# Optimization experiments

Measured on AMD Instinct MI355X. Metric: run time of the kernel, lower is better.

## Reference

```python
import jax, jax.numpy as jnp
import numpy as np

B = 4096
D = 256
N = 9000000
ALPHA = 0.5      # alpha_weight
GAMMA_S = 0.8
GAMMA_U = 0.9
RHO = 6.0
EPS = 1e-14
ETA = 0.01
TAU_MIN = 0.001
TAU_MAX = 1.0
GRAD_CLIP = 5.0
TAU_INIT = 0.07


def setup_inputs() -> dict:
    key = jax.random.key(0)
    k1, k2 = jax.random.split(key)
    return {
        "zis": jax.random.normal(k1, (B, D), dtype=jnp.float32),
        "zjs": jax.random.normal(k2, (B, D), dtype=jnp.float32),
        "ids": jnp.arange(B, dtype=jnp.int32),
        "s_I": jnp.zeros(N, jnp.float32),
        "s_T": jnp.zeros(N, jnp.float32),
        "b_I": jnp.zeros(N, jnp.float32),
        "b_T": jnp.zeros(N, jnp.float32),
        "u_I": jnp.zeros(N, jnp.float32),
        "u_T": jnp.zeros(N, jnp.float32),
        "tau_I": jnp.full(N, TAU_INIT, jnp.float32),
        "tau_T": jnp.full(N, TAU_INIT, jnp.float32),
    }


def reference(zis, zjs, ids, s_I, s_T, b_I, b_T, u_I, u_T, tau_I, tau_T):
    sg = jax.lax.stop_gradient
    Bc = zis.shape[0]
    # normalize
    zis = zis / jnp.linalg.norm(zis, axis=1, keepdims=True)
    zjs = zjs / jnp.linalg.norm(zjs, axis=1, keepdims=True)
    sim = jnp.einsum('id,jd->ij', zis, zjs)                 # [B,B]
    diag = jnp.diagonal(sim)
    image_diffs = sim - diag[:, None]
    text_diffs = sim - diag[None, :]
    tau_i = tau_I[ids]
    tau_t = tau_T[ids]
    # detached temperature-scaled diffs (torch .detach())
    idt = sg(image_diffs) / tau_i[:, None]
    tdt = sg(text_diffs) / tau_t[None, :]
    # running max update (online log-sum-exp shift)
    old_b_i = b_I[ids]
    old_b_t = b_T[ids]
    new_b_i = jnp.maximum(old_b_i, idt.max(axis=1))
    new_b_t = jnp.maximum(old_b_t, tdt.max(axis=0))
    mask = 1.0 - jnp.eye(Bc, dtype=zis.dtype)
    exp_i = jnp.exp(idt - new_b_i[:, None]) * mask
    exp_t = jnp.exp(tdt - new_b_t[None, :]) * mask
    g_i = exp_i.sum(axis=1)                                  # [B]
    g_t = exp_t.sum(axis=0)                                  # [B]
    # EMA of normalizers, rescaled by max shift
    s_i = (1.0 - GAMMA_S) * s_I[ids] * jnp.exp(old_b_i - new_b_i) + GAMMA_S * g_i
    s_t = (1.0 - GAMMA_S) * s_T[ids] * jnp.exp(old_b_t - new_b_t) + GAMMA_S * g_t
    s_i_c = jnp.clip(s_i, EPS, None)[:, None]                # [B,1]
    s_t_c = jnp.clip(s_t, EPS, None)[None, :]                # [1,B]
    w_i = exp_i / s_i_c
    w_t = exp_t / s_t_c
    image_loss = (sg(w_i) * image_diffs).sum(axis=1)         # [B]
    text_loss = (sg(w_t) * text_diffs).sum(axis=0)           # [B]
    total_loss = ALPHA * image_loss.mean() + (1.0 - ALPHA) * text_loss.mean()
    grad_tau_image = jnp.log(s_i_c) + new_b_i[:, None] + RHO - (w_i * idt).sum(axis=1, keepdims=True) / (Bc - 1)
    grad_tau_text = jnp.log(s_t_c) + new_b_t[None, :] + RHO - (w_t * tdt).sum(axis=0, keepdims=True) / (Bc - 1)
    # EMA of tau gradients with clipping, then temperature update
    u_i = (1.0 - GAMMA_U) * u_I[ids] + GAMMA_U * jnp.clip(grad_tau_image[:, 0], -GRAD_CLIP, GRAD_CLIP)
    u_t = (1.0 - GAMMA_U) * u_T[ids] + GAMMA_U * jnp.clip(grad_tau_text[0, :], -GRAD_CLIP, GRAD_CLIP)
    tau_i_new = jnp.clip(tau_i - ETA * u_i, TAU_MIN, TAU_MAX)
    tau_t_new = jnp.clip(tau_t - ETA * u_t, TAU_MIN, TAU_MAX)
    # scatter updated state back into persistent buffers
    s_I = s_I.at[ids].set(s_i)
    s_T = s_T.at[ids].set(s_t)
    b_I = b_I.at[ids].set(new_b_i)
    b_T = b_T.at[ids].set(new_b_t)
    u_I = u_I.at[ids].set(u_i)
    u_T = u_T.at[ids].set(u_t)
    tau_I = tau_I.at[ids].set(tau_i_new)
    tau_T = tau_T.at[ids].set(tau_t_new)
    return (g_i[:, None], g_t[None, :], grad_tau_image, grad_tau_text, total_loss,
            tau_i.mean(), tau_t.mean(), s_I, s_T, b_I, b_T, u_I, u_T, tau_I, tau_T)
```

## Files before the change

### kernel.cpp

```cpp
#include <hip/hip_runtime.h>
#include <math.h>

#define BDIM 4096
#define DDIM 256
#define NSTATE 9000000

#define C_ALPHA 0.5f
#define C_GAMMA_S 0.8f
#define C_GAMMA_U 0.9f
#define C_RHO 6.0f
#define C_EPS 1e-14f
#define C_ETA 0.01f
#define C_TAU_MIN 0.001f
#define C_TAU_MAX 1.0f
#define C_GRAD_CLIP 5.0f

typedef unsigned short u16;
typedef __attribute__((ext_vector_type(8))) short short8;
typedef __attribute__((ext_vector_type(16))) float f32x16;

#define MFMA32 __builtin_amdgcn_mfma_f32_32x32x16_bf16

__device__ inline u16 f2bf(float f) {
    unsigned u = __float_as_uint(f);
    unsigned r = (u + 0x7FFFu + ((u >> 16) & 1u)) >> 16;
    return (u16)r;
}
__device__ inline float bf2f(u16 h) { return __uint_as_float(((unsigned)h) << 16); }

__global__ __launch_bounds__(256) void ktau(const int* __restrict__ ids,
                                            const float* __restrict__ tau_I,
                                            const float* __restrict__ tau_T,
                                            float* __restrict__ rowIT,
                                            float* __restrict__ colIT) {
    int i = blockIdx.x * 256 + threadIdx.x;
    if (i >= BDIM) return;
    int id = ids[i];
    rowIT[i] = 1.0f / tau_I[id];
    colIT[i] = 1.0f / tau_T[id];
}

__global__ __launch_bounds__(256) void kprep(const float* __restrict__ zis,
                                             const float* __restrict__ zjs,
                                             u16* __restrict__ Ah, u16* __restrict__ Al,
                                             u16* __restrict__ Bh, u16* __restrict__ Bl) {
    int blk = blockIdx.x;
    bool isB = blk >= 128;
    const float* Z = isB ? zjs : zis;
    u16* H = isB ? Bh : Ah;
    u16* L = isB ? Bl : Al;
    int rblk = blk & 127;
    int t = threadIdx.x;
    int r = t & 31, kc0 = t >> 5;
    int row = rblk * 32 + r;

    __shared__ float ssq[32];
    if (t < 32) ssq[t] = 0.f;
    __syncthreads();

    float4 v[8];
    float partial = 0.f;
#pragma unroll
    for (int c = 0; c < 4; ++c) {
        int kc = kc0 + 8 * c;
        float4 a = *(const float4*)&Z[(size_t)row * DDIM + kc * 8];
        float4 b = *(const float4*)&Z[(size_t)row * DDIM + kc * 8 + 4];
        v[2 * c] = a; v[2 * c + 1] = b;
        partial += a.x * a.x + a.y * a.y + a.z * a.z + a.w * a.w;
        partial += b.x * b.x + b.y * b.y + b.z * b.z + b.w * b.w;
    }
    atomicAdd(&ssq[r], partial);
    __syncthreads();
    float inv = rsqrtf(ssq[r]);

#pragma unroll
    for (int c = 0; c < 4; ++c) {
        int kc = kc0 + 8 * c;
        float f[8];
        f[0] = v[2*c].x * inv;   f[1] = v[2*c].y * inv;
        f[2] = v[2*c].z * inv;   f[3] = v[2*c].w * inv;
        f[4] = v[2*c+1].x * inv; f[5] = v[2*c+1].y * inv;
        f[6] = v[2*c+1].z * inv; f[7] = v[2*c+1].w * inv;
        u16 hh[8], ll[8];
#pragma unroll
        for (int j = 0; j < 8; ++j) {
            hh[j] = f2bf(f[j]);
            ll[j] = f2bf(f[j] - bf2f(hh[j]));
        }
        size_t base = (size_t)rblk * 8192 + (size_t)kc * 256 + (size_t)r * 8;
        uint4 ph, pl;
        ph.x = (unsigned)hh[0] | ((unsigned)hh[1] << 16);
        ph.y = (unsigned)hh[2] | ((unsigned)hh[3] << 16);
        ph.z = (unsigned)hh[4] | ((unsigned)hh[5] << 16);
        ph.w = (unsigned)hh[6] | ((unsigned)hh[7] << 16);
        pl.x = (unsigned)ll[0] | ((unsigned)ll[1] << 16);
        pl.y = (unsigned)ll[2] | ((unsigned)ll[3] << 16);
        pl.z = (unsigned)ll[4] | ((unsigned)ll[5] << 16);
        pl.w = (unsigned)ll[6] | ((unsigned)ll[7] << 16);
        *(uint4*)(H + base) = ph;
        *(uint4*)(L + base) = pl;
    }
}

__global__ __launch_bounds__(256, 3) void kgemm(
    const u16* __restrict__ Ah, const u16* __restrict__ Al,
    const u16* __restrict__ Bh, const u16* __restrict__ Bl,
    const float* __restrict__ rowIT, const float* __restrict__ colIT,
    float* __restrict__ rPM, float* __restrict__ rPS1, float* __restrict__ rPS2,
    float* __restrict__ cPM, float* __restrict__ cPS1, float* __restrict__ cPS2,
    float* __restrict__ diag)
{
    __shared__ float T[2][64 * 68];

    int bx = blockIdx.x, by = blockIdx.y;
    int t = threadIdx.x;
    int w = t >> 6, l = t & 63;
    int rw = w & 1, cw = w >> 1;
    int h = l >> 5, lc = l & 31;
    int rowbase = by * 128 + rw * 64;
    int colbase = bx * 128 + cw * 64;

    const u16* pAh = Ah + (size_t)(by * 4 + rw * 2) * 8192;
    const u16* pAl = Al + (size_t)(by * 4 + rw * 2) * 8192;
    const u16* pBh = Bh + (size_t)(bx * 4 + cw * 2) * 8192;
    const u16* pBl = Bl + (size_t)(bx * 4 + cw * 2) * 8192;

    f32x16 acc00, acc01, acc10, acc11;
#pragma unroll
    for (int e = 0; e < 16; ++e) { acc00[e] = 0.f; acc01[e] = 0.f; acc10[e] = 0.f; acc11[e] = 0.f; }

    for (int s = 0; s < 16; ++s) {
        int off = s * 512 + l * 8;
        short8 a0h = *(const short8*)(pAh + off);
        short8 a1h = *(const short8*)(pAh + 8192 + off);
        short8 a0l = *(const short8*)(pAl + off);
        short8 a1l = *(const short8*)(pAl + 8192 + off);
        short8 b0h = *(const short8*)(pBh + off);
        short8 b1h = *(const short8*)(pBh + 8192 + off);
        short8 b0l = *(const short8*)(pBl + off);
        short8 b1l = *(const short8*)(pBl + 8192 + off);

        acc00 = MFMA32(a0h, b0h, acc00, 0, 0, 0);
        acc01 = MFMA32(a0h, b1h, acc01, 0, 0, 0);
        acc10 = MFMA32(a1h, b0h, acc10, 0, 0, 0);
        acc11 = MFMA32(a1h, b1h, acc11, 0, 0, 0);
        acc00 = MFMA32(a0h, b0l, acc00, 0, 0, 0);
        acc01 = MFMA32(a0h, b1l, acc01, 0, 0, 0);
        acc10 = MFMA32(a1h, b0l, acc10, 0, 0, 0);
        acc11 = MFMA32(a1h, b1l, acc11, 0, 0, 0);
        acc00 = MFMA32(a0l, b0h, acc00, 0, 0, 0);
        acc01 = MFMA32(a0l, b1h, acc01, 0, 0, 0);
        acc10 = MFMA32(a1l, b0h, acc10, 0, 0, 0);
        acc11 = MFMA32(a1l, b1h, acc11, 0, 0, 0);
    }

#define COLPART(A0, A1, CT) do {                                                   \
        int gc = colbase + (CT) * 32 + lc;                                         \
        float itc = colIT[gc];                                                     \
        float m = -INFINITY;                                                       \
        _Pragma("unroll") for (int e = 0; e < 16; ++e) {                           \
            m = fmaxf(m, (A0)[e]); m = fmaxf(m, (A1)[e]); }                        \
        m = fmaxf(m, __shfl_xor(m, 32));                                           \
        float S1 = 0.f, S2 = 0.f;                                                  \
        _Pragma("unroll") for (int e = 0; e < 16; ++e) {                           \
            float v0 = (A0)[e]; float e0 = __expf((v0 - m) * itc); S1 += e0; S2 += e0 * v0; \
            float v1 = (A1)[e]; float e1 = __expf((v1 - m) * itc); S1 += e1; S2 += e1 * v1; } \
        S1 += __shfl_xor(S1, 32); S2 += __shfl_xor(S2, 32);                        \
        if (h == 0) { int slot = by * 2 + rw;                                      \
            cPM [slot * 4096 + gc] = m;                                            \
            cPS1[slot * 4096 + gc] = S1;                                           \
            cPS2[slot * 4096 + gc] = S2; }                                         \
    } while (0)

    COLPART(acc00, acc10, 0);
    COLPART(acc01, acc11, 1);

#define ROWPART(TB) do {                                                           \
        float* Tb = (TB);                                                          \
        _Pragma("unroll") for (int q = 0; q < 4; ++q) {                            \
            _Pragma("unroll") for (int j = 0; j < 4; ++j) {                        \
                int rr = 8 * q + 4 * h + j;                                        \
                Tb[(rr     ) * 68 + lc     ] = acc00[4 * q + j];                   \
                Tb[(rr     ) * 68 + lc + 32] = acc01[4 * q + j];                   \
                Tb[(rr + 32) * 68 + lc     ] = acc10[4 * q + j];                   \
                Tb[(rr + 32) * 68 + lc + 32] = acc11[4 * q + j]; } }               \
        float itr = rowIT[rowbase + l];                                            \
        float4 vv[16];                                                             \
        _Pragma("unroll") for (int c = 0; c < 16; ++c)                             \
            vv[c] = *(const float4*)&Tb[l * 68 + 4 * c];                           \
        float m = -INFINITY;                                                       \
        _Pragma("unroll") for (int c = 0; c < 16; ++c)                             \
            m = fmaxf(m, fmaxf(fmaxf(vv[c].x, vv[c].y), fmaxf(vv[c].z, vv[c].w))); \
        float S1 = 0.f, S2 = 0.f;                                                  \
        _Pragma("unroll") for (int c = 0; c < 16; ++c) {                           \
            float e0 = __expf((vv[c].x - m) * itr); S1 += e0; S2 += e0 * vv[c].x;  \
            float e1 = __expf((vv[c].y - m) * itr); S1 += e1; S2 += e1 * vv[c].y;  \
            float e2 = __expf((vv[c].z - m) * itr); S1 += e2; S2 += e2 * vv[c].z;  \
            float e3 = __expf((vv[c].w - m) * itr); S1 += e3; S2 += e3 * vv[c].w; }\
        int slot = bx * 2 + cw;                                                    \
        rPM [slot * 4096 + rowbase + l] = m;                                       \
        rPS1[slot * 4096 + rowbase + l] = S1;                                      \
        rPS2[slot * 4096 + rowbase + l] = S2;                                      \
        if (bx == by && rw == cw) diag[rowbase + l] = Tb[l * 68 + l];              \
    } while (0)

    if (w < 2) ROWPART(T[w]);
    __syncthreads();
    if (w >= 2) ROWPART(T[w - 2]);
}

__global__ __launch_bounds__(256) void kmerge(
    const int* __restrict__ ids,
    const float* __restrict__ s_I, const float* __restrict__ b_I,
    const float* __restrict__ u_I, const float* __restrict__ tau_I,
    const float* __restrict__ s_T, const float* __restrict__ b_T,
    const float* __restrict__ u_T, const float* __restrict__ tau_T,
    const float* __restrict__ rowIT, const float* __restrict__ colIT,
    const float* __restrict__ diag,
    const float* __restrict__ rPM, const float* __restrict__ rPS1, const float* __restrict__ rPS2,
    const float* __restrict__ cPM, const float* __restrict__ cPS1, const float* __restrict__ cPS2,
    float* __restrict__ O,
    float* __restrict__ sc_arrs,
    float* __restrict__ img_loss_arr,
    float* __restrict__ txt_loss_arr)
{
    int j = blockIdx.x * 256 + threadIdx.x;
    if (j >= 2 * BDIM) return;
    bool rowside = (j < BDIM);
    int i = rowside ? j : j - BDIM;
    const float* PM  = rowside ? rPM  : cPM;
    const float* PS1 = rowside ? rPS1 : cPS1;
    const float* PS2 = rowside ? rPS2 : cPS2;
    float it = rowside ? rowIT[i] : colIT[i];

    float M = -INFINITY, S1 = 0.f, S2 = 0.f;
    for (int k = 0; k < 64; k++) {
        float m  = PM [k * BDIM + i];
        float s1 = PS1[k * BDIM + i];
        float s2 = PS2[k * BDIM + i];
        float Mn = fmaxf(M, m);
        float ea = __expf((M - Mn) * it);
        float eb = __expf((m - Mn) * it);
        S1 = S1 * ea + s1 * eb;
        S2 = S2 * ea + s2 * eb;
        M = Mn;
    }

    int id = ids[i];
    float tau  = rowside ? tau_I[id] : tau_T[id];
    float oldb = rowside ? b_I[id]   : b_T[id];
    float olds = rowside ? s_I[id]   : s_T[id];
    float oldu = rowside ? u_I[id]   : u_T[id];
    float dg = diag[i];

    float nb = fmaxf(oldb, (M - dg) * it);
    float F  = __expf((M - dg) * it - nb);
    float ed = __expf(-nb);
    float g  = F * S1 - ed;
    float Cs = F * (S2 - dg * S1);

    float s_new = (1.f - C_GAMMA_S) * olds * __expf(oldb - nb) + C_GAMMA_S * g;
    float sc = fmaxf(s_new, C_EPS);
    float loss = Cs / sc;
    float grad = logf(sc) + nb + C_RHO - (Cs / (sc * tau)) * (1.0f / (float)(BDIM - 1));
    float gc = fminf(fmaxf(grad, -C_GRAD_CLIP), C_GRAD_CLIP);
    float u_new = (1.f - C_GAMMA_U) * oldu + C_GAMMA_U * gc;
    float tau_new = fminf(fmaxf(tau - C_ETA * u_new, C_TAU_MIN), C_TAU_MAX);

    if (rowside) {
        O[i] = g;
        O[8192 + i] = grad;
        sc_arrs[0 * BDIM + i] = s_new;
        sc_arrs[1 * BDIM + i] = nb;
        sc_arrs[2 * BDIM + i] = u_new;
        sc_arrs[3 * BDIM + i] = tau_new;
        img_loss_arr[i] = loss;
    } else {
        O[4096 + i] = g;
        O[12288 + i] = grad;
        sc_arrs[4 * BDIM + i] = s_new;
        sc_arrs[5 * BDIM + i] = nb;
        sc_arrs[6 * BDIM + i] = u_new;
        sc_arrs[7 * BDIM + i] = tau_new;
        txt_loss_arr[i] = loss;
    }
}

__global__ __launch_bounds__(256) void kscalars(const float* __restrict__ img_loss_arr,
                                                const float* __restrict__ txt_loss_arr,
                                                const int* __restrict__ ids,
                                                const float* __restrict__ tau_I,
                                                const float* __restrict__ tau_T,
                                                float* __restrict__ O) {
    int t = threadIdx.x;
    float s0 = 0.f, s1 = 0.f, s2 = 0.f, s3 = 0.f;
    for (int k = t; k < BDIM; k += 256) {
        s0 += img_loss_arr[k];
        s1 += txt_loss_arr[k];
        int id = ids[k];
        s2 += tau_I[id];
        s3 += tau_T[id];
    }
    __shared__ float r0[256], r1[256], r2[256], r3[256];
    r0[t] = s0; r1[t] = s1; r2[t] = s2; r3[t] = s3;
    __syncthreads();
    for (int s = 128; s > 0; s >>= 1) {
        if (t < s) {
            r0[t] += r0[t + s]; r1[t] += r1[t + s];
            r2[t] += r2[t + s]; r3[t] += r3[t + s];
        }
        __syncthreads();
    }
    if (t == 0) {
        float invB = 1.0f / (float)BDIM;
        O[16384] = C_ALPHA * (r0[0] * invB) + (1.f - C_ALPHA) * (r1[0] * invB);
        O[16385] = r2[0] * invB;
        O[16386] = r3[0] * invB;
    }
}

__global__ __launch_bounds__(256) void kcopy(const float* __restrict__ s_I,
                                             const float* __restrict__ s_T,
                                             const float* __restrict__ b_I,
                                             const float* __restrict__ b_T,
                                             const float* __restrict__ u_I,
                                             const float* __restrict__ u_T,
                                             const float* __restrict__ tau_I,
                                             const float* __restrict__ tau_T,
                                             float* __restrict__ o) {
    const float4* srcs[8] = {(const float4*)s_I, (const float4*)s_T,
                             (const float4*)b_I, (const float4*)b_T,
                             (const float4*)u_I, (const float4*)u_T,
                             (const float4*)tau_I, (const float4*)tau_T};
    long tid = (long)blockIdx.x * 256 + threadIdx.x;
#pragma unroll
    for (int b = 0; b < 8; b++) {
        const float4* s = srcs[b];
        float* d = o + (long)b * NSTATE;
        for (long k = tid; k < NSTATE / 4; k += 2097152) {
            float4 v = s[k];
            float* dp = d + 4 * k;
            dp[0] = v.x; dp[1] = v.y; dp[2] = v.z; dp[3] = v.w;
        }
    }
}

__global__ __launch_bounds__(256) void kscatter(const int* __restrict__ ids,
                                                const float* __restrict__ sc_arrs,
                                                float* __restrict__ o) {
    int t = blockIdx.x * 256 + threadIdx.x;
    if (t >= BDIM) return;
    long id = ids[t];
    o[0L * NSTATE + id] = sc_arrs[0 * BDIM + t];
    o[1L * NSTATE + id] = sc_arrs[4 * BDIM + t];
    o[2L * NSTATE + id] = sc_arrs[1 * BDIM + t];
    o[3L * NSTATE + id] = sc_arrs[5 * BDIM + t];
    o[4L * NSTATE + id] = sc_arrs[2 * BDIM + t];
    o[5L * NSTATE + id] = sc_arrs[6 * BDIM + t];
    o[6L * NSTATE + id] = sc_arrs[3 * BDIM + t];
    o[7L * NSTATE + id] = sc_arrs[7 * BDIM + t];
}

extern "C" void kernel_launch(void* const* d_in, const int* in_sizes, int n_in,
                              void* d_out, int out_size, void* d_ws, size_t ws_size,
                              hipStream_t stream) {
    const float* zis   = (const float*)d_in[0];
    const float* zjs   = (const float*)d_in[1];
    const int*   ids   = (const int*)d_in[2];
    const float* s_I   = (const float*)d_in[3];
    const float* s_T   = (const float*)d_in[4];
    const float* b_I   = (const float*)d_in[5];
    const float* b_T   = (const float*)d_in[6];
    const float* u_I   = (const float*)d_in[7];
    const float* u_T   = (const float*)d_in[8];
    const float* tau_I = (const float*)d_in[9];
    const float* tau_T = (const float*)d_in[10];
    float* O  = (float*)d_out;
    float* ws = (float*)d_ws;

    float* P = O + 16388;
    float* rPM  = P;
    float* rPS1 = P + 262144;
    float* rPS2 = P + 524288;
    float* cPM  = P + 786432;
    float* cPS1 = P + 1048576;
    float* cPS2 = P + 1310720;
    float* diag = P + 1572864;
    u16* AB = (u16*)(P + 1576960);
    u16* Ah = AB;
    u16* Al = AB + 1048576;
    u16* Bh = AB + 2097152;
    u16* Bl = AB + 3145728;

    float* rowIT  = ws;
    float* colIT  = ws + 4096;
    float* sc_arrs = ws + 8192;
    float* img_loss_arr = ws + 40960;
    float* txt_loss_arr = ws + 45056;

    ktau<<<16, 256, 0, stream>>>(ids, tau_I, tau_T, rowIT, colIT);
    kprep<<<256, 256, 0, stream>>>(zis, zjs, Ah, Al, Bh, Bl);

    kgemm<<<dim3(32, 32), 256, 0, stream>>>(Ah, Al, Bh, Bl, rowIT, colIT,
                                            rPM, rPS1, rPS2, cPM, cPS1, cPS2, diag);

    kmerge<<<32, 256, 0, stream>>>(ids, s_I, b_I, u_I, tau_I, s_T, b_T, u_T, tau_T,
                                   rowIT, colIT, diag,
                                   rPM, rPS1, rPS2, cPM, cPS1, cPS2,
                                   O, sc_arrs, img_loss_arr, txt_loss_arr);

    kscalars<<<1, 256, 0, stream>>>(img_loss_arr, txt_loss_arr, ids, tau_I, tau_T, O);

    kcopy<<<8192, 256, 0, stream>>>(s_I, s_T, b_I, b_T, u_I, u_T, tau_I, tau_T, O + 16387);

    kscatter<<<16, 256, 0, stream>>>(ids, sc_arrs, O + 16387);
}
```

Before: 557.0 us.

## Overlap state-buffer copy with GEMM by interleaving copy blocks into its grid

The bulk copy of the eight persistent state buffers moves into the GEMM launch. Four out of every five blocks run a nontemporal float4 copy, and the rest compute GEMM tiles, so the memory-bound copy can overlap the compute-bound matmul. The part of s_I whose output region also serves as scratch for the GEMM partials is copied later, in a kernel fused with the scalar reduction. The tau-reciprocal kernel is folded into kprep as an extra block, which cuts launch count. The risk is that the copy blocks compete with GEMM blocks for bandwidth and occupancy.

```diff
diff --git a/kernel.cpp b/kernel.cpp
--- a/kernel.cpp
+++ b/kernel.cpp
@@ -4,6 +4,10 @@
 #define BDIM 4096
 #define DDIM 256
 #define NSTATE 9000000
+#define PREFIX 3674116
+#define BANK0_N4 1331471
+#define PREFIX_N4 918529
+#define COPY_THREADS 1048576
 
 #define C_ALPHA 0.5f
 #define C_GAMMA_S 0.8f
@@ -18,6 +22,7 @@
 typedef unsigned short u16;
 typedef __attribute__((ext_vector_type(8))) short short8;
 typedef __attribute__((ext_vector_type(16))) float f32x16;
+typedef __attribute__((ext_vector_type(4))) float nf4;
 
 #define MFMA32 __builtin_amdgcn_mfma_f32_32x32x16_bf16
 
@@ -28,29 +33,39 @@
 }
 __device__ inline float bf2f(u16 h) { return __uint_as_float(((unsigned)h) << 16); }
 
-__global__ __launch_bounds__(256) void ktau(const int* __restrict__ ids,
-                                            const float* __restrict__ tau_I,
-                                            const float* __restrict__ tau_T,
-                                            float* __restrict__ rowIT,
-                                            float* __restrict__ colIT) {
-    int i = blockIdx.x * 256 + threadIdx.x;
-    if (i >= BDIM) return;
-    int id = ids[i];
-    rowIT[i] = 1.0f / tau_I[id];
-    colIT[i] = 1.0f / tau_T[id];
+__device__ inline void nt_copy4(const nf4* __restrict__ s, long k, float* __restrict__ dbase) {
+    nf4 v = __builtin_nontemporal_load(&s[k]);
+    float* dp = dbase + 4 * k;
+    __builtin_nontemporal_store(v.x, dp + 0);
+    __builtin_nontemporal_store(v.y, dp + 1);
+    __builtin_nontemporal_store(v.z, dp + 2);
+    __builtin_nontemporal_store(v.w, dp + 3);
 }
 
 __global__ __launch_bounds__(256) void kprep(const float* __restrict__ zis,
                                              const float* __restrict__ zjs,
                                              u16* __restrict__ Ah, u16* __restrict__ Al,
-                                             u16* __restrict__ Bh, u16* __restrict__ Bl) {
+                                             u16* __restrict__ Bh, u16* __restrict__ Bl,
+                                             const int* __restrict__ ids,
+                                             const float* __restrict__ tau_I,
+                                             const float* __restrict__ tau_T,
+                                             float* __restrict__ rowIT,
+                                             float* __restrict__ colIT) {
     int blk = blockIdx.x;
+    int t = threadIdx.x;
+    if (blk == 256) {
+        for (int i = t; i < BDIM; i += 256) {
+            int id = ids[i];
+            rowIT[i] = 1.0f / tau_I[id];
+            colIT[i] = 1.0f / tau_T[id];
+        }
+        return;
+    }
     bool isB = blk >= 128;
     const float* Z = isB ? zjs : zis;
     u16* H = isB ? Bh : Ah;
     u16* L = isB ? Bl : Al;
     int rblk = blk & 127;
-    int t = threadIdx.x;
     int r = t & 31, kc0 = t >> 5;
     int row = rblk * 32 + r;
 
@@ -102,18 +117,43 @@
     }
 }
 
-__global__ __launch_bounds__(256, 3) void kgemm(
+__global__ __launch_bounds__(256, 3) void kmain(
     const u16* __restrict__ Ah, const u16* __restrict__ Al,
     const u16* __restrict__ Bh, const u16* __restrict__ Bl,
     const float* __restrict__ rowIT, const float* __restrict__ colIT,
     float* __restrict__ rPM, float* __restrict__ rPS1, float* __restrict__ rPS2,
     float* __restrict__ cPM, float* __restrict__ cPS1, float* __restrict__ cPS2,
-    float* __restrict__ diag)
+    float* __restrict__ diag,
+    const float* __restrict__ s_I, const float* __restrict__ s_T,
+    const float* __restrict__ b_I, const float* __restrict__ b_T,
+    const float* __restrict__ u_I, const float* __restrict__ u_T,
+    const float* __restrict__ tau_I, const float* __restrict__ tau_T,
+    float* o)
 {
     __shared__ float T[2][64 * 68];
-
-    int bx = blockIdx.x, by = blockIdx.y;
+    int bid = blockIdx.x;
     int t = threadIdx.x;
+
+    if (bid % 5 != 0) {
+        long cid = (long)(bid / 5) * 4 + (bid % 5) - 1;
+        long tid = cid * 256 + t;
+        {
+            const nf4* s = (const nf4*)(s_I + PREFIX);
+            float* d = o + PREFIX;
+            for (long k = tid; k < BANK0_N4; k += COPY_THREADS) nt_copy4(s, k, d);
+        }
+        const float* srcs[7] = {s_T, b_I, b_T, u_I, u_T, tau_I, tau_T};
+#pragma unroll
+        for (int b = 0; b < 7; b++) {
+            const nf4* s = (const nf4*)srcs[b];
+            float* d = o + (long)(b + 1) * NSTATE;
+            for (long k = tid; k < NSTATE / 4; k += COPY_THREADS) nt_copy4(s, k, d);
+        }
+        return;
+    }
+
+    int gid = bid / 5;
+    int by = gid >> 5, bx = gid & 31;
     int w = t >> 6, l = t & 63;
     int rw = w & 1, cw = w >> 1;
     int h = l >> 5, lc = l & 31;
@@ -286,13 +326,20 @@
     }
 }
 
-__global__ __launch_bounds__(256) void kscalars(const float* __restrict__ img_loss_arr,
-                                                const float* __restrict__ txt_loss_arr,
-                                                const int* __restrict__ ids,
-                                                const float* __restrict__ tau_I,
-                                                const float* __restrict__ tau_T,
-                                                float* __restrict__ O) {
+__global__ __launch_bounds__(256) void kfix(const float* s_I, float* o,
+                                            const float* img_loss_arr,
+                                            const float* txt_loss_arr,
+                                            const int* ids,
+                                            const float* tau_I, const float* tau_T,
+                                            float* O) {
+    int bid = blockIdx.x;
     int t = threadIdx.x;
+    if (bid < 3584) {
+        long tid = (long)bid * 256 + t;
+        const nf4* s = (const nf4*)s_I;
+        for (long k = tid; k < PREFIX_N4; k += 3584L * 256) nt_copy4(s, k, o);
+        return;
+    }
     float s0 = 0.f, s1 = 0.f, s2 = 0.f, s3 = 0.f;
     for (int k = t; k < BDIM; k += 256) {
         s0 += img_loss_arr[k];
@@ -319,35 +366,9 @@
     }
 }
 
-__global__ __launch_bounds__(256) void kcopy(const float* __restrict__ s_I,
-                                             const float* __restrict__ s_T,
-                                             const float* __restrict__ b_I,
-                                             const float* __restrict__ b_T,
-                                             const float* __restrict__ u_I,
-                                             const float* __restrict__ u_T,
-                                             const float* __restrict__ tau_I,
-                                             const float* __restrict__ tau_T,
+__global__ __launch_bounds__(256) void kscat(const int* __restrict__ ids,
+                                             const float* __restrict__ sc_arrs,
                                              float* __restrict__ o) {
-    const float4* srcs[8] = {(const float4*)s_I, (const float4*)s_T,
-                             (const float4*)b_I, (const float4*)b_T,
-                             (const float4*)u_I, (const float4*)u_T,
-                             (const float4*)tau_I, (const float4*)tau_T};
-    long tid = (long)blockIdx.x * 256 + threadIdx.x;
-#pragma unroll
-    for (int b = 0; b < 8; b++) {
-        const float4* s = srcs[b];
-        float* d = o + (long)b * NSTATE;
-        for (long k = tid; k < NSTATE / 4; k += 2097152) {
-            float4 v = s[k];
-            float* dp = d + 4 * k;
-            dp[0] = v.x; dp[1] = v.y; dp[2] = v.z; dp[3] = v.w;
-        }
-    }
-}
-
-__global__ __launch_bounds__(256) void kscatter(const int* __restrict__ ids,
-                                                const float* __restrict__ sc_arrs,
-                                                float* __restrict__ o) {
     int t = blockIdx.x * 256 + threadIdx.x;
     if (t >= BDIM) return;
     long id = ids[t];
@@ -398,20 +419,21 @@
     float* img_loss_arr = ws + 40960;
     float* txt_loss_arr = ws + 45056;
 
-    ktau<<<16, 256, 0, stream>>>(ids, tau_I, tau_T, rowIT, colIT);
-    kprep<<<256, 256, 0, stream>>>(zis, zjs, Ah, Al, Bh, Bl);
-
-    kgemm<<<dim3(32, 32), 256, 0, stream>>>(Ah, Al, Bh, Bl, rowIT, colIT,
-                                            rPM, rPS1, rPS2, cPM, cPS1, cPS2, diag);
+    kprep<<<257, 256, 0, stream>>>(zis, zjs, Ah, Al, Bh, Bl,
+                                   ids, tau_I, tau_T, rowIT, colIT);
+
+    kmain<<<5120, 256, 0, stream>>>(Ah, Al, Bh, Bl, rowIT, colIT,
+                                    rPM, rPS1, rPS2, cPM, cPS1, cPS2, diag,
+                                    s_I, s_T, b_I, b_T, u_I, u_T, tau_I, tau_T,
+                                    O + 16387);
 
     kmerge<<<32, 256, 0, stream>>>(ids, s_I, b_I, u_I, tau_I, s_T, b_T, u_T, tau_T,
                                    rowIT, colIT, diag,
                                    rPM, rPS1, rPS2, cPM, cPS1, cPS2,
                                    O, sc_arrs, img_loss_arr, txt_loss_arr);
 
-    kscalars<<<1, 256, 0, stream>>>(img_loss_arr, txt_loss_arr, ids, tau_I, tau_T, O);
-
-    kcopy<<<8192, 256, 0, stream>>>(s_I, s_T, b_I, b_T, u_I, u_T, tau_I, tau_T, O + 16387);
-
-    kscatter<<<16, 256, 0, stream>>>(ids, sc_arrs, O + 16387);
-}
+    kfix<<<3585, 256, 0, stream>>>(s_I, O + 16387, img_loss_arr, txt_loss_arr,
+                                   ids, tau_I, tau_T, O);
+
+    kscat<<<16, 256, 0, stream>>>(ids, sc_arrs, O + 16387);
+}
```

Result: no change. 552.4 us (-0.8%).
